# Performance work log

Measured on AMD Instinct MI355X. Metric: run time of the kernel, lower is better.

Reference implementation:

```python
import jax, jax.numpy as jnp
import numpy as np

N_NODES = 100000
N_EDGES = 1_600_000
N_ROIS = 400
HIDDEN = 128
N_GRAPHS = 512
OUT = 2


def setup_inputs() -> dict:
    key = jax.random.key(0)
    ks = jax.random.split(key, 7)
    x = jax.random.normal(ks[0], (N_NODES, N_ROIS), dtype=jnp.float32)
    edge_index = jax.random.randint(ks[1], (2, N_EDGES), 0, N_NODES, dtype=jnp.int32)
    # sorted graph-assignment vector; prepend arange so every graph id is non-empty
    rnd = jax.random.randint(ks[2], (N_NODES - N_GRAPHS,), 0, N_GRAPHS, dtype=jnp.int32)
    batch = jnp.sort(jnp.concatenate([jnp.arange(N_GRAPHS, dtype=jnp.int32), rnd]))
    W = jax.random.normal(ks[3], (N_ROIS, HIDDEN), dtype=jnp.float32) / np.float32(np.sqrt(N_ROIS))
    b = jnp.zeros((HIDDEN,), dtype=jnp.float32)
    lin_W = jax.random.normal(ks[4], (HIDDEN, OUT), dtype=jnp.float32) / np.float32(np.sqrt(HIDDEN))
    lin_b = jnp.zeros((OUT,), dtype=jnp.float32)
    return {"x": x, "edge_index": edge_index, "batch": batch,
            "W": W, "b": b, "lin_W": lin_W, "lin_b": lin_b}


def reference(x, edge_index, batch, W, b, lin_W, lin_b):
    N = x.shape[0]
    # GCNConv: add self-loops, symmetric normalization D^-1/2 (A+I) D^-1/2
    loops = jnp.arange(N, dtype=edge_index.dtype)
    row = jnp.concatenate([edge_index[0], loops])  # source
    col = jnp.concatenate([edge_index[1], loops])  # target
    deg = jax.ops.segment_sum(jnp.ones_like(col, dtype=x.dtype), col, num_segments=N)
    dinv = jnp.where(deg > 0, jax.lax.rsqrt(deg), 0.0)
    norm = dinv[row] * dinv[col]                   # [E+N]
    h = x @ W                                      # [N, H] transform before propagate
    msg = h[row] * norm[:, None]                   # [E+N, H]
    agg = jax.ops.segment_sum(msg, col, num_segments=N) + b
    act = jax.nn.relu(agg)                         # [N, H]
    # global max pool over graph ids (all segments guaranteed non-empty)
    pooled = jax.ops.segment_max(act, batch, num_segments=N_GRAPHS)  # [G, H]
    logits = pooled @ lin_W + lin_b                # [G, OUT]
    return logits, pooled
```

## Files before the change

kernel.cpp:

```cpp
#include <hip/hip_runtime.h>
#include <hip/hip_bf16.h>

#define N_NODES 100000
#define N_EDGES 1600000
#define N_ROIS  400
#define RKP     416
#define HID     128
#define N_GRAPHS 512
#define NOUT    2
#define NBUCK   391
#define BCAP    8192
#define ECH     4096
#define NPW     16

typedef __attribute__((ext_vector_type(8))) short short8;
typedef __attribute__((ext_vector_type(4))) float f32x4;

static __device__ __forceinline__ unsigned short f2bf(float f) {
  unsigned u = __float_as_uint(f);
  u += 0x7fffu + ((u >> 16) & 1u);
  return (unsigned short)(u >> 16);
}
static __device__ __forceinline__ float bf2f(unsigned short h) {
  return __uint_as_float(((unsigned)h) << 16);
}

__global__ __launch_bounds__(256) void bucket_k(
    const int* __restrict__ row, const int* __restrict__ col,
    int* __restrict__ bcnt, unsigned int* __restrict__ pairs) {
  __shared__ int hist[NBUCK];
  __shared__ int base[NBUCK];
  int t = threadIdx.x;
  for (int b = t; b < NBUCK; b += 256) hist[b] = 0;
  __syncthreads();
  int e0 = blockIdx.x * ECH;
  unsigned int pk[16];
  int bk[16], rk[16];
#pragma unroll
  for (int i = 0; i < 16; ++i) {
    int e = e0 + t + i * 256;
    if (e < N_EDGES) {
      int r = row[e], c = col[e];
      bk[i] = c >> 8;
      pk[i] = ((unsigned)r << 8) | (unsigned)(c & 255);
      rk[i] = atomicAdd(&hist[bk[i]], 1);
    } else bk[i] = -1;
  }
  __syncthreads();
  for (int b = t; b < NBUCK; b += 256)
    base[b] = (hist[b] > 0) ? atomicAdd(&bcnt[b], hist[b]) : 0;
  __syncthreads();
#pragma unroll
  for (int i = 0; i < 16; ++i)
    if (bk[i] >= 0) {
      int p = base[bk[i]] + rk[i];
      if (p < BCAP) pairs[(size_t)bk[i] * BCAP + p] = pk[i];
    }
}

__global__ __launch_bounds__(256) void csr_build_k(
    const unsigned int* __restrict__ pairs, const int* __restrict__ bcnt,
    int* __restrict__ csr_row, int* __restrict__ offs, int* __restrict__ cnt,
    float* __restrict__ dinv) {
  __shared__ unsigned int ep[BCAP];
  __shared__ int h[256];
  __shared__ int sc[256];
  __shared__ int cur[256];
  int b = blockIdx.x;
  int t = threadIdx.x;
  int m = min(bcnt[b], BCAP);
  size_t base = (size_t)b * BCAP;
  for (int j = t; j < m; j += 256) ep[j] = pairs[base + j];
  h[t] = 0;
  __syncthreads();
  for (int j = t; j < m; j += 256) atomicAdd(&h[ep[j] & 255u], 1);
  __syncthreads();
  int myc = h[t];
  sc[t] = myc;
  __syncthreads();
  for (int off = 1; off < 256; off <<= 1) {
    int v = (t >= off) ? sc[t - off] : 0;
    __syncthreads();
    sc[t] += v;
    __syncthreads();
  }
  int loff = sc[t] - myc;
  cur[t] = loff;
  int node = b * 256 + t;
  if (node < N_NODES) {
    cnt[node] = myc;
    offs[node] = (int)base + loff;
    dinv[node] = rsqrtf((float)(myc + 1));
  }
  __syncthreads();
  for (int j = t; j < m; j += 256) {
    unsigned int e = ep[j];
    int pos = atomicAdd(&cur[e & 255u], 1);
    csr_row[base + pos] = (int)(e >> 8);
  }
}

__global__ void prep_wt_k(const float* __restrict__ W, unsigned short* __restrict__ Wt) {
  int idx = blockIdx.x * blockDim.x + threadIdx.x;
  if (idx < HID * RKP) {
    int n = idx / RKP, k = idx - n * RKP;
    float v = (k < N_ROIS) ? W[k * HID + n] : 0.f;
    Wt[idx] = f2bf(v);
  }
}

__global__ __launch_bounds__(256) void gemm_k(
    const float* __restrict__ x, const unsigned short* __restrict__ Wt,
    const float* __restrict__ dinv, unsigned short* __restrict__ hp) {
  __shared__ __align__(16) short As[64][40];
  __shared__ __align__(16) short Bs[HID][40];
  int t = threadIdx.x;
  int lane = t & 63;
  int wv = t >> 6;
  int row0 = blockIdx.x * 64;
  int mrow = lane & 15;
  int kgrp = lane >> 4;

  f32x4 acc[8];
#pragma unroll
  for (int i = 0; i < 8; ++i) acc[i] = (f32x4){0.f, 0.f, 0.f, 0.f};

  int arow = t >> 2;
  int akofs = (t & 3) * 8;
  int brow = t >> 1;
  int bkofs = (t & 1) * 16;
  int grow_a = row0 + arow;
  const float* xp = x + (size_t)grow_a * N_ROIS;

  for (int kk = 0; kk < RKP; kk += 32) {
    short8 a8;
    if (grow_a < N_NODES && kk + akofs + 8 <= N_ROIS) {
      float4 f0 = *(const float4*)(xp + kk + akofs);
      float4 f1 = *(const float4*)(xp + kk + akofs + 4);
      a8[0] = (short)f2bf(f0.x); a8[1] = (short)f2bf(f0.y);
      a8[2] = (short)f2bf(f0.z); a8[3] = (short)f2bf(f0.w);
      a8[4] = (short)f2bf(f1.x); a8[5] = (short)f2bf(f1.y);
      a8[6] = (short)f2bf(f1.z); a8[7] = (short)f2bf(f1.w);
    } else {
#pragma unroll
      for (int u = 0; u < 8; ++u) {
        int k = kk + akofs + u;
        float f = (grow_a < N_NODES && k < N_ROIS) ? xp[k] : 0.f;
        a8[u] = (short)f2bf(f);
      }
    }
    *(short8*)&As[arow][akofs] = a8;
    const short8* wp = (const short8*)(Wt + (size_t)brow * RKP + kk + bkofs);
    *(short8*)&Bs[brow][bkofs] = wp[0];
    *(short8*)&Bs[brow][bkofs + 8] = wp[1];
    __syncthreads();

    short8 af = *(const short8*)&As[wv * 16 + mrow][kgrp * 8];
#pragma unroll
    for (int nt = 0; nt < 8; ++nt) {
      short8 bf = *(const short8*)&Bs[nt * 16 + mrow][kgrp * 8];
      acc[nt] = __builtin_amdgcn_mfma_f32_16x16x32_bf16(af, bf, acc[nt], 0, 0, 0);
    }
    __syncthreads();
  }

#pragma unroll
  for (int r = 0; r < 4; ++r) {
    int grow = row0 + wv * 16 + kgrp * 4 + r;
    if (grow < N_NODES) {
      float di = dinv[grow];
      unsigned short* op = hp + (size_t)grow * HID + mrow;
#pragma unroll
      for (int nt = 0; nt < 8; ++nt) {
        op[nt * 16] = f2bf(di * acc[nt][r]);
      }
    }
  }
}

__global__ __launch_bounds__(256) void gather_k(
    const unsigned short* __restrict__ hp, const int* __restrict__ csr_row,
    const int* __restrict__ offs, const int* __restrict__ cnt,
    const float* __restrict__ dinv, const int* __restrict__ batch,
    const float* __restrict__ bias, unsigned int* __restrict__ pooled_bits) {
  int wave = (blockIdx.x * blockDim.x + threadIdx.x) >> 6;
  int lane = threadIdx.x & 63;
  int n0 = wave * NPW;
  if (n0 >= N_NODES) return;
  int nend = min(n0 + NPW, N_NODES);
  float2 bb = *(const float2*)(bias + lane * 2);
  float rm0 = 0.f, rm1 = 0.f;
  int cur_g = batch[n0];

  for (int i = n0; i < nend; ++i) {
    int start = offs[i];
    int m = cnt[i];
    unsigned int u = *(const unsigned int*)(hp + (size_t)i * HID + lane * 2);
    float ax = bf2f((unsigned short)(u & 0xffff));
    float ay = bf2f((unsigned short)(u >> 16));
    int j = 0;
    for (; j + 4 <= m; j += 4) {
      int s0 = csr_row[start + j];
      int s1 = csr_row[start + j + 1];
      int s2 = csr_row[start + j + 2];
      int s3 = csr_row[start + j + 3];
      unsigned int u0 = *(const unsigned int*)(hp + (size_t)s0 * HID + lane * 2);
      unsigned int u1 = *(const unsigned int*)(hp + (size_t)s1 * HID + lane * 2);
      unsigned int u2 = *(const unsigned int*)(hp + (size_t)s2 * HID + lane * 2);
      unsigned int u3 = *(const unsigned int*)(hp + (size_t)s3 * HID + lane * 2);
      ax += (bf2f((unsigned short)(u0 & 0xffff)) + bf2f((unsigned short)(u1 & 0xffff)))
          + (bf2f((unsigned short)(u2 & 0xffff)) + bf2f((unsigned short)(u3 & 0xffff)));
      ay += (bf2f((unsigned short)(u0 >> 16)) + bf2f((unsigned short)(u1 >> 16)))
          + (bf2f((unsigned short)(u2 >> 16)) + bf2f((unsigned short)(u3 >> 16)));
    }
    for (; j < m; ++j) {
      int s0 = csr_row[start + j];
      unsigned int u0 = *(const unsigned int*)(hp + (size_t)s0 * HID + lane * 2);
      ax += bf2f((unsigned short)(u0 & 0xffff));
      ay += bf2f((unsigned short)(u0 >> 16));
    }
    float di = dinv[i];
    float p0 = fmaxf(fmaf(di, ax, bb.x), 0.f);
    float p1 = fmaxf(fmaf(di, ay, bb.y), 0.f);
    int g = batch[i];
    if (g != cur_g) {
      atomicMax(&pooled_bits[cur_g * HID + lane * 2],     __float_as_uint(rm0));
      atomicMax(&pooled_bits[cur_g * HID + lane * 2 + 1], __float_as_uint(rm1));
      rm0 = 0.f; rm1 = 0.f;
      cur_g = g;
    }
    rm0 = fmaxf(rm0, p0);
    rm1 = fmaxf(rm1, p1);
  }
  atomicMax(&pooled_bits[cur_g * HID + lane * 2],     __float_as_uint(rm0));
  atomicMax(&pooled_bits[cur_g * HID + lane * 2 + 1], __float_as_uint(rm1));
}

__global__ void logits_k(const float* __restrict__ pooled, const float* __restrict__ lin_W,
                         const float* __restrict__ lin_b, float* __restrict__ out) {
  int t = blockIdx.x * blockDim.x + threadIdx.x;
  if (t < N_GRAPHS * NOUT) {
    int g = t >> 1, o = t & 1;
    float s = lin_b[o];
    const float* pg = pooled + g * HID;
#pragma unroll 8
    for (int k = 0; k < HID; ++k) s = fmaf(pg[k], lin_W[k * NOUT + o], s);
    out[t] = s;
  }
}

extern "C" void kernel_launch(void* const* d_in, const int* in_sizes, int n_in,
                              void* d_out, int out_size, void* d_ws, size_t ws_size,
                              hipStream_t stream) {
  (void)in_sizes; (void)n_in; (void)ws_size;
  const float* x     = (const float*)d_in[0];
  const int*   ei    = (const int*)d_in[1];
  const int*   row   = ei;
  const int*   col   = ei + N_EDGES;
  const int*   batch = (const int*)d_in[2];
  const float* W     = (const float*)d_in[3];
  const float* b     = (const float*)d_in[4];
  const float* lin_W = (const float*)d_in[5];
  const float* lin_b = (const float*)d_in[6];
  float* out = (float*)d_out;

  char* ws = (char*)d_ws;
  int*   bcnt    = (int*)(ws + 0);
  int*   offs    = (int*)(ws + 4096);
  int*   cnt     = (int*)(ws + 404096);
  float* dinv    = (float*)(ws + 804096);
  unsigned short* Wt = (unsigned short*)(ws + 1204096);
  int*   csr_row = (int*)(ws + 1310720);
  unsigned int* pairs = (unsigned int*)(ws + 14123008);
  unsigned short* hp  = (unsigned short*)(ws + 14123008);

  hipMemsetAsync(bcnt, 0, NBUCK * sizeof(int), stream);
  hipMemsetAsync(d_out, 0, (size_t)out_size * sizeof(float), stream);

  bucket_k<<<(N_EDGES + ECH - 1) / ECH, 256, 0, stream>>>(row, col, bcnt, pairs);
  csr_build_k<<<NBUCK, 256, 0, stream>>>(pairs, bcnt, csr_row, offs, cnt, dinv);
  prep_wt_k<<<(HID * RKP + 255) / 256, 256, 0, stream>>>(W, Wt);
  gemm_k<<<(N_NODES + 63) / 64, 256, 0, stream>>>(x, Wt, dinv, hp);
  {
    int waves = (N_NODES + NPW - 1) / NPW;
    int blocks = (waves * 64 + 255) / 256;
    gather_k<<<blocks, 256, 0, stream>>>(
        hp, csr_row, offs, cnt, dinv, batch, b,
        (unsigned int*)(out + N_GRAPHS * NOUT));
  }
  logits_k<<<(N_GRAPHS * NOUT + 255) / 256, 256, 0, stream>>>(
      out + N_GRAPHS * NOUT, lin_W, lin_b, out);
}
```

Measured before the change: 391.4 us.

## Stream W tiles via direct global-to-LDS loads and widen gather to 16-byte rows

The GEMM no longer stages x through shared memory. Each lane loads its A fragment straight from global memory and converts it in registers. The W tiles are double-buffered into LDS with global_load_lds so the next k-slice loads while the MFMAs run. The gather kernel switches to 16 lanes per row with 8 bf16 values each (uint4 loads), splits each node's neighbours across 4 lane groups and reduces them with cross-lane shuffles. The aim is to cut LDS traffic and syncs in the GEMM and issue fewer, wider memory transactions in the gather, at the cost of shuffle work and atomics limited to one quarter of the wave.

```diff
diff --git a/kernel.cpp b/kernel.cpp
--- a/kernel.cpp
+++ b/kernel.cpp
@@ -21,8 +21,16 @@
   u += 0x7fffu + ((u >> 16) & 1u);
   return (unsigned short)(u >> 16);
 }
-static __device__ __forceinline__ float bf2f(unsigned short h) {
-  return __uint_as_float(((unsigned)h) << 16);
+static __device__ __forceinline__ float blo(unsigned int u) {
+  return __uint_as_float(u << 16);
+}
+static __device__ __forceinline__ float bhi(unsigned int u) {
+  return __uint_as_float(u & 0xffff0000u);
+}
+static __device__ __forceinline__ void gl2lds16(const void* g, void* l) {
+  __builtin_amdgcn_global_load_lds(
+      (const __attribute__((address_space(1))) unsigned int*)g,
+      (__attribute__((address_space(3))) unsigned int*)l, 16, 0, 0);
 }
 
 __global__ __launch_bounds__(256) void bucket_k(
@@ -112,8 +120,7 @@
 __global__ __launch_bounds__(256) void gemm_k(
     const float* __restrict__ x, const unsigned short* __restrict__ Wt,
     const float* __restrict__ dinv, unsigned short* __restrict__ hp) {
-  __shared__ __align__(16) short As[64][40];
-  __shared__ __align__(16) short Bs[HID][40];
+  __shared__ __align__(16) unsigned short Bs[2][512 * 8];
   int t = threadIdx.x;
   int lane = t & 63;
   int wv = t >> 6;
@@ -121,44 +128,47 @@
   int mrow = lane & 15;
   int kgrp = lane >> 4;
 
+  int n_a = t & 127, kg_a = t >> 7;
+  const unsigned short* wsrc0 = Wt + (size_t)n_a * RKP + kg_a * 8;
+  const unsigned short* wsrc1 = wsrc0 + 16;
+  unsigned short* ldst0 = &Bs[0][(size_t)wv * 64 * 8];
+  unsigned short* ldst1 = ldst0 + 256 * 8;
+
+  int grow_r = row0 + wv * 16 + mrow;
+  const float* xp = x + (size_t)min(grow_r, N_NODES - 1) * N_ROIS + kgrp * 8;
+
   f32x4 acc[8];
 #pragma unroll
   for (int i = 0; i < 8; ++i) acc[i] = (f32x4){0.f, 0.f, 0.f, 0.f};
 
-  int arow = t >> 2;
-  int akofs = (t & 3) * 8;
-  int brow = t >> 1;
-  int bkofs = (t & 1) * 16;
-  int grow_a = row0 + arow;
-  const float* xp = x + (size_t)grow_a * N_ROIS;
-
-  for (int kk = 0; kk < RKP; kk += 32) {
-    short8 a8;
-    if (grow_a < N_NODES && kk + akofs + 8 <= N_ROIS) {
-      float4 f0 = *(const float4*)(xp + kk + akofs);
-      float4 f1 = *(const float4*)(xp + kk + akofs + 4);
-      a8[0] = (short)f2bf(f0.x); a8[1] = (short)f2bf(f0.y);
-      a8[2] = (short)f2bf(f0.z); a8[3] = (short)f2bf(f0.w);
-      a8[4] = (short)f2bf(f1.x); a8[5] = (short)f2bf(f1.y);
-      a8[6] = (short)f2bf(f1.z); a8[7] = (short)f2bf(f1.w);
+  gl2lds16(wsrc0, ldst0);
+  gl2lds16(wsrc1, ldst1);
+  __syncthreads();
+
+  for (int s = 0; s < 13; ++s) {
+    int kk = s * 32;
+    short8 af;
+    if (kk + kgrp * 8 < N_ROIS) {
+      float4 f0 = *(const float4*)(xp + kk);
+      float4 f1 = *(const float4*)(xp + kk + 4);
+      af[0] = (short)f2bf(f0.x); af[1] = (short)f2bf(f0.y);
+      af[2] = (short)f2bf(f0.z); af[3] = (short)f2bf(f0.w);
+      af[4] = (short)f2bf(f1.x); af[5] = (short)f2bf(f1.y);
+      af[6] = (short)f2bf(f1.z); af[7] = (short)f2bf(f1.w);
     } else {
 #pragma unroll
-      for (int u = 0; u < 8; ++u) {
-        int k = kk + akofs + u;
-        float f = (grow_a < N_NODES && k < N_ROIS) ? xp[k] : 0.f;
-        a8[u] = (short)f2bf(f);
-      }
-    }
-    *(short8*)&As[arow][akofs] = a8;
-    const short8* wp = (const short8*)(Wt + (size_t)brow * RKP + kk + bkofs);
-    *(short8*)&Bs[brow][bkofs] = wp[0];
-    *(short8*)&Bs[brow][bkofs + 8] = wp[1];
-    __syncthreads();
-
-    short8 af = *(const short8*)&As[wv * 16 + mrow][kgrp * 8];
+      for (int u = 0; u < 8; ++u) af[u] = 0;
+    }
+    if (s < 12) {
+      int nb = (s + 1) & 1;
+      unsigned short* d0 = &Bs[nb][(size_t)wv * 64 * 8];
+      gl2lds16(wsrc0 + (kk + 32), d0);
+      gl2lds16(wsrc1 + (kk + 32), d0 + 256 * 8);
+    }
+    const unsigned short* bb = &Bs[s & 1][0];
 #pragma unroll
     for (int nt = 0; nt < 8; ++nt) {
-      short8 bf = *(const short8*)&Bs[nt * 16 + mrow][kgrp * 8];
+      short8 bf = *(const short8*)&bb[(size_t)(kgrp * 128 + nt * 16 + mrow) * 8];
       acc[nt] = __builtin_amdgcn_mfma_f32_16x16x32_bf16(af, bf, acc[nt], 0, 0, 0);
     }
     __syncthreads();
@@ -185,55 +195,70 @@
     const float* __restrict__ bias, unsigned int* __restrict__ pooled_bits) {
   int wave = (blockIdx.x * blockDim.x + threadIdx.x) >> 6;
   int lane = threadIdx.x & 63;
+  int q = lane >> 4;
+  int d = lane & 15;
   int n0 = wave * NPW;
   if (n0 >= N_NODES) return;
   int nend = min(n0 + NPW, N_NODES);
-  float2 bb = *(const float2*)(bias + lane * 2);
-  float rm0 = 0.f, rm1 = 0.f;
+  float4 bb0 = *(const float4*)(bias + d * 8);
+  float4 bb1 = *(const float4*)(bias + d * 8 + 4);
+  float rm[8];
+#pragma unroll
+  for (int k = 0; k < 8; ++k) rm[k] = 0.f;
   int cur_g = batch[n0];
 
   for (int i = n0; i < nend; ++i) {
     int start = offs[i];
     int m = cnt[i];
-    unsigned int u = *(const unsigned int*)(hp + (size_t)i * HID + lane * 2);
-    float ax = bf2f((unsigned short)(u & 0xffff));
-    float ay = bf2f((unsigned short)(u >> 16));
-    int j = 0;
-    for (; j + 4 <= m; j += 4) {
-      int s0 = csr_row[start + j];
-      int s1 = csr_row[start + j + 1];
-      int s2 = csr_row[start + j + 2];
-      int s3 = csr_row[start + j + 3];
-      unsigned int u0 = *(const unsigned int*)(hp + (size_t)s0 * HID + lane * 2);
-      unsigned int u1 = *(const unsigned int*)(hp + (size_t)s1 * HID + lane * 2);
-      unsigned int u2 = *(const unsigned int*)(hp + (size_t)s2 * HID + lane * 2);
-      unsigned int u3 = *(const unsigned int*)(hp + (size_t)s3 * HID + lane * 2);
-      ax += (bf2f((unsigned short)(u0 & 0xffff)) + bf2f((unsigned short)(u1 & 0xffff)))
-          + (bf2f((unsigned short)(u2 & 0xffff)) + bf2f((unsigned short)(u3 & 0xffff)));
-      ay += (bf2f((unsigned short)(u0 >> 16)) + bf2f((unsigned short)(u1 >> 16)))
-          + (bf2f((unsigned short)(u2 >> 16)) + bf2f((unsigned short)(u3 >> 16)));
-    }
-    for (; j < m; ++j) {
-      int s0 = csr_row[start + j];
-      unsigned int u0 = *(const unsigned int*)(hp + (size_t)s0 * HID + lane * 2);
-      ax += bf2f((unsigned short)(u0 & 0xffff));
-      ay += bf2f((unsigned short)(u0 >> 16));
+    float a[8];
+    if (q == 0) {
+      uint4 u = *(const uint4*)(hp + (size_t)i * HID + d * 8);
+      a[0] = blo(u.x); a[1] = bhi(u.x); a[2] = blo(u.y); a[3] = bhi(u.y);
+      a[4] = blo(u.z); a[5] = bhi(u.z); a[6] = blo(u.w); a[7] = bhi(u.w);
+    } else {
+#pragma unroll
+      for (int k = 0; k < 8; ++k) a[k] = 0.f;
+    }
+    for (int j = q; j < m; j += 4) {
+      int s = csr_row[start + j];
+      uint4 u = *(const uint4*)(hp + (size_t)s * HID + d * 8);
+      a[0] += blo(u.x); a[1] += bhi(u.x); a[2] += blo(u.y); a[3] += bhi(u.y);
+      a[4] += blo(u.z); a[5] += bhi(u.z); a[6] += blo(u.w); a[7] += bhi(u.w);
+    }
+#pragma unroll
+    for (int k = 0; k < 8; ++k) {
+      a[k] += __shfl_xor(a[k], 16, 64);
+      a[k] += __shfl_xor(a[k], 32, 64);
     }
     float di = dinv[i];
-    float p0 = fmaxf(fmaf(di, ax, bb.x), 0.f);
-    float p1 = fmaxf(fmaf(di, ay, bb.y), 0.f);
+    float p[8];
+    p[0] = fmaxf(fmaf(di, a[0], bb0.x), 0.f);
+    p[1] = fmaxf(fmaf(di, a[1], bb0.y), 0.f);
+    p[2] = fmaxf(fmaf(di, a[2], bb0.z), 0.f);
+    p[3] = fmaxf(fmaf(di, a[3], bb0.w), 0.f);
+    p[4] = fmaxf(fmaf(di, a[4], bb1.x), 0.f);
+    p[5] = fmaxf(fmaf(di, a[5], bb1.y), 0.f);
+    p[6] = fmaxf(fmaf(di, a[6], bb1.z), 0.f);
+    p[7] = fmaxf(fmaf(di, a[7], bb1.w), 0.f);
     int g = batch[i];
     if (g != cur_g) {
-      atomicMax(&pooled_bits[cur_g * HID + lane * 2],     __float_as_uint(rm0));
-      atomicMax(&pooled_bits[cur_g * HID + lane * 2 + 1], __float_as_uint(rm1));
-      rm0 = 0.f; rm1 = 0.f;
+      if (q == 0) {
+#pragma unroll
+        for (int k = 0; k < 8; ++k)
+          atomicMax(&pooled_bits[cur_g * HID + d * 8 + k], __float_as_uint(rm[k]));
+      }
+#pragma unroll
+      for (int k = 0; k < 8; ++k) rm[k] = 0.f;
       cur_g = g;
     }
-    rm0 = fmaxf(rm0, p0);
-    rm1 = fmaxf(rm1, p1);
-  }
-  atomicMax(&pooled_bits[cur_g * HID + lane * 2],     __float_as_uint(rm0));
-  atomicMax(&pooled_bits[cur_g * HID + lane * 2 + 1], __float_as_uint(rm1));
+#pragma unroll
+    for (int k = 0; k < 8; ++k) rm[k] = fmaxf(rm[k], p[k]);
+  }
+  if (q == 0) {
+#pragma unroll
+    for (int k = 0; k < 8; ++k)
+      atomicMax(&pooled_bits[cur_g * HID + d * 8 + k], __float_as_uint(rm[k]));
+  }
 }
 
 __global__ void logits_k(const float* __restrict__ pooled, const float* __restrict__ lin_W,
```

Measured after the change: 403.2 us. 1.03x slower.
